# Kernel tuning notes

Hardware: AMD Instinct MI355X
Metric: run time of the kernel (lower is better)

Reference implementation:

```python
import jax, jax.numpy as jnp
import numpy as np

D_MODEL = 1024
NUM_HEADS = 16
D_HEAD = D_MODEL // NUM_HEADS
LN_EPS = 1e-5


def setup_inputs() -> dict:
    key = jax.random.key(0)
    ks = jax.random.split(key, 10)
    s = 1.0 / np.sqrt(D_MODEL)
    inp = {
        "batch": jax.random.normal(ks[0], (4, 2048, D_MODEL), dtype=jnp.float32),
        "wq": jax.random.uniform(ks[1], (D_MODEL, D_MODEL), jnp.float32, -s, s),
        "bq": jax.random.uniform(ks[2], (D_MODEL,), jnp.float32, -s, s),
        "wk": jax.random.uniform(ks[3], (D_MODEL, D_MODEL), jnp.float32, -s, s),
        "bk": jax.random.uniform(ks[4], (D_MODEL,), jnp.float32, -s, s),
        "wv": jax.random.uniform(ks[5], (D_MODEL, D_MODEL), jnp.float32, -s, s),
        "bv": jax.random.uniform(ks[6], (D_MODEL,), jnp.float32, -s, s),
        "wo": jax.random.uniform(ks[7], (D_MODEL, D_MODEL), jnp.float32, -s, s),
        "bo": jax.random.uniform(ks[8], (D_MODEL,), jnp.float32, -s, s),
        "ln_g": jnp.ones((D_MODEL,), jnp.float32),
        "ln_b": jnp.zeros((D_MODEL,), jnp.float32),
    }
    return inp


def reference(batch, wq, bq, wk, bk, wv, bv, wo, bo, ln_g, ln_b):
    B, S, D = batch.shape
    # QKV projections (torch Linear: x @ W.T + b)
    q = (batch @ wq.T + bq).reshape(B, S, NUM_HEADS, D_HEAD)
    k = (batch @ wk.T + bk).reshape(B, S, NUM_HEADS, D_HEAD)
    v = (batch @ wv.T + bv).reshape(B, S, NUM_HEADS, D_HEAD)
    # attention scores [B, H, S, S]
    scores = jnp.einsum("bqhd,bkhd->bhqk", q, k) / np.sqrt(D_HEAD).astype(np.float32)
    # (original masked_fill is not in-place -> mask has no effect; omitted)
    probs = jax.nn.softmax(scores, axis=-1)
    attn = jnp.einsum("bhqk,bkhd->bqhd", probs, v).reshape(B, S, D)
    residual = attn @ wo.T + bo  # dropout = identity (eval mode)
    x = batch + residual
    mu = jnp.mean(x, axis=-1, keepdims=True)
    var = jnp.mean(jnp.square(x - mu), axis=-1, keepdims=True)
    return (x - mu) / jnp.sqrt(var + LN_EPS) * ln_g + ln_b
```

## Files before the change

kernel.cpp:

```cpp
#include <hip/hip_runtime.h>

typedef __bf16 bf16_t;
typedef __bf16 v8bf __attribute__((ext_vector_type(8)));
typedef __bf16 v4bf __attribute__((ext_vector_type(4)));
typedef float  v4f  __attribute__((ext_vector_type(4)));

#define D_MODEL 1024
#define NHEAD   16
#define DHEAD   64
#define SEQ     2048
#define BATCH   4
#define ROWS    (BATCH*SEQ)

#define GLD16(g, l) __builtin_amdgcn_global_load_lds( \
    (const __attribute__((address_space(1))) void*)(g), \
    (__attribute__((address_space(3))) void*)(l), 16, 0, 0)

__global__ __launch_bounds__(256) void k_prep(const float* __restrict__ batch,
                                              const float* __restrict__ wq,
                                              const float* __restrict__ wk,
                                              const float* __restrict__ wv,
                                              const float* __restrict__ wo,
                                              const float* __restrict__ bq,
                                              const float* __restrict__ bk,
                                              const float* __restrict__ bv,
                                              bf16_t* __restrict__ Xb,
                                              bf16_t* __restrict__ Wqkv,
                                              bf16_t* __restrict__ Wob,
                                              float* __restrict__ bqkv) {
    int bid = blockIdx.x, t = threadIdx.x;
    const float* src; bf16_t* dst; int idx;
    if (bid < 8192)       { src = batch; dst = Xb;             idx = bid * 256 + t; }
    else if (bid < 9216)  { src = wq;    dst = Wqkv;           idx = (bid - 8192) * 256 + t; }
    else if (bid < 10240) { src = wk;    dst = Wqkv + 1048576; idx = (bid - 9216) * 256 + t; }
    else if (bid < 11264) { src = wv;    dst = Wqkv + 2097152; idx = (bid - 10240) * 256 + t; }
    else if (bid < 12288) { src = wo;    dst = Wob;            idx = (bid - 11264) * 256 + t; }
    else {
        int i = (bid - 12288) * 256 + t;
        if (i < 1024) bqkv[i] = bq[i];
        else if (i < 2048) bqkv[i] = bk[i - 1024];
        else if (i < 3072) bqkv[i] = bv[i - 2048];
        return;
    }
    float4 f = ((const float4*)src)[idx];
    v4bf o;
    o[0] = (bf16_t)f.x; o[1] = (bf16_t)f.y; o[2] = (bf16_t)f.z; o[3] = (bf16_t)f.w;
    ((v4bf*)dst)[idx] = o;
}

__global__ __launch_bounds__(256, 3) void k_gemm_bt(
    const bf16_t* __restrict__ A, const bf16_t* __restrict__ Bm,
    const float* __restrict__ bias, const float* __restrict__ resid,
    bf16_t* __restrict__ Cb, float* __restrict__ Cf,
    int M, int N, int K, int qcols, float qmul)
{
    __shared__ bf16_t As[2][128 * 32];
    __shared__ bf16_t Bs[2][128 * 32];

    int nTile = N >> 7;
    int m0 = (blockIdx.x / nTile) << 7;
    int n0 = (blockIdx.x % nTile) << 7;
    int t = threadIdx.x;
    int w = t >> 6, lane = t & 63, quad = lane >> 4, ln = lane & 15;
    int wm = (w >> 1) << 6, wn = (w & 1) << 6;

    int srow = lane >> 2;
    int scol = ((lane & 3) ^ ((lane >> 3) & 3)) << 3;
    const bf16_t* Ag0 = A  + (size_t)(m0 + w * 16 +      srow) * K + scol;
    const bf16_t* Ag1 = A  + (size_t)(m0 + w * 16 + 64 + srow) * K + scol;
    const bf16_t* Bg0 = Bm + (size_t)(n0 + w * 16 +      srow) * K + scol;
    const bf16_t* Bg1 = Bm + (size_t)(n0 + w * 16 + 64 + srow) * K + scol;
    int lo0 = (w * 16) * 32, lo1 = (w * 16 + 64) * 32;

    v4f acc[4][4];
#pragma unroll
    for (int i = 0; i < 4; i++)
#pragma unroll
        for (int j = 0; j < 4; j++) acc[i][j] = (v4f){0.f, 0.f, 0.f, 0.f};

    GLD16(Ag0, &As[0][lo0]);
    GLD16(Ag1, &As[0][lo1]);
    GLD16(Bg0, &Bs[0][lo0]);
    GLD16(Bg1, &Bs[0][lo1]);

    int sw = (ln >> 1) & 3;
    int buf = 0;
    for (int k0 = 0; k0 < K; k0 += 32, buf ^= 1) {
        __syncthreads();
        if (k0 + 32 < K) {
            GLD16(Ag0 + k0 + 32, &As[buf ^ 1][lo0]);
            GLD16(Ag1 + k0 + 32, &As[buf ^ 1][lo1]);
            GLD16(Bg0 + k0 + 32, &Bs[buf ^ 1][lo0]);
            GLD16(Bg1 + k0 + 32, &Bs[buf ^ 1][lo1]);
        }
        v8bf af[4], bfr[4];
#pragma unroll
        for (int mt = 0; mt < 4; mt++)
            af[mt] = *(const v8bf*)&As[buf][(wm + mt * 16 + ln) * 32 + ((quad ^ sw) << 3)];
#pragma unroll
        for (int nt = 0; nt < 4; nt++)
            bfr[nt] = *(const v8bf*)&Bs[buf][(wn + nt * 16 + ln) * 32 + ((quad ^ sw) << 3)];
#pragma unroll
        for (int mt = 0; mt < 4; mt++)
#pragma unroll
            for (int nt = 0; nt < 4; nt++)
                acc[mt][nt] = __builtin_amdgcn_mfma_f32_16x16x32_bf16(af[mt], bfr[nt], acc[mt][nt], 0, 0, 0);
    }

#pragma unroll
    for (int mt = 0; mt < 4; mt++) {
#pragma unroll
        for (int r = 0; r < 4; r++) {
            int row = m0 + wm + mt * 16 + quad * 4 + r;
#pragma unroll
            for (int nt = 0; nt < 4; nt++) {
                int col = n0 + wn + nt * 16 + ln;
                float v = acc[mt][nt][r] + bias[col];
                if (Cf) Cf[(size_t)row * N + col] = v + resid[(size_t)row * N + col];
                else {
                    if (col < qcols) v *= qmul;
                    Cb[(size_t)row * N + col] = (bf16_t)v;
                }
            }
        }
    }
}

__global__ __launch_bounds__(256) void k_transpose_v(const bf16_t* __restrict__ qkv,
                                                     bf16_t* __restrict__ vt) {
    __shared__ bf16_t tile[64 * 72];
    int bid = blockIdx.x;
    int st = bid & 31, bh = bid >> 5, b = bh >> 4, h = bh & 15;
    int t = threadIdx.x;
    const bf16_t* src = qkv + (size_t)(b * SEQ + st * 64) * 3072 + 2048 + h * 64;
#pragma unroll
    for (int i = 0; i < 2; i++) {
        int c = t + i * 256, row = c >> 3, c8 = (c & 7) << 3;
        *(uint4*)&tile[row * 72 + c8] = *(const uint4*)(src + (size_t)row * 3072 + c8);
    }
    __syncthreads();
    bf16_t* dst = vt + (size_t)bh * DHEAD * SEQ + st * 64;
#pragma unroll
    for (int i = 0; i < 2; i++) {
        int c = t + i * 256, d = c >> 3, s8 = (c & 7) << 3;
        v8bf o;
#pragma unroll
        for (int j = 0; j < 8; j++) o[j] = tile[(s8 + j) * 72 + d];
        *(v8bf*)(dst + (size_t)d * SEQ + s8) = o;
    }
}

__global__ __launch_bounds__(256, 3) void k_attn(const bf16_t* __restrict__ qkv,
                                                 const bf16_t* __restrict__ vt,
                                                 bf16_t* __restrict__ attn) {
    __shared__ bf16_t Ks[2][64 * 64];
    __shared__ bf16_t Vs[2][64 * 64];
    __shared__ bf16_t Pl[4][16 * 64];

    int bid = blockIdx.x;
    int qt = bid & 15, bh = bid >> 4, b = bh >> 4, h = bh & 15;
    int t = threadIdx.x, w = t >> 6, lane = t & 63, quad = lane >> 4, ln = lane & 15;
    int q0 = qt * 128 + w * 32;

    v8bf qf[2][2];
#pragma unroll
    for (int qs = 0; qs < 2; qs++) {
        const bf16_t* Qp = qkv + (size_t)(b * SEQ + q0 + qs * 16 + ln) * 3072 + h * 64 + quad * 8;
        qf[qs][0] = *(const v8bf*)Qp;
        qf[qs][1] = *(const v8bf*)(Qp + 32);
    }

    int srow = lane >> 3;
    int scol = ((lane & 7) ^ (lane >> 3)) << 3;
    const bf16_t* Kg0 = qkv + (size_t)(b * SEQ + w * 8 +      srow) * 3072 + 1024 + h * 64 + scol;
    const bf16_t* Kg1 = qkv + (size_t)(b * SEQ + w * 8 + 32 + srow) * 3072 + 1024 + h * 64 + scol;
    const bf16_t* Vg0 = vt + (size_t)bh * DHEAD * SEQ + (size_t)(w * 8 +      srow) * SEQ + scol;
    const bf16_t* Vg1 = vt + (size_t)bh * DHEAD * SEQ + (size_t)(w * 8 + 32 + srow) * SEQ + scol;
    int ko0 = (w * 8) * 64, ko1 = (w * 8 + 32) * 64;

    bf16_t* Pw = &Pl[w][0];
    int swv = ln & 7;

    v4f o[2][4];
#pragma unroll
    for (int qs = 0; qs < 2; qs++)
#pragma unroll
        for (int d = 0; d < 4; d++) o[qs][d] = (v4f){0.f, 0.f, 0.f, 0.f};
    float lsum[2][4] = {{0.f,0.f,0.f,0.f},{0.f,0.f,0.f,0.f}};

    GLD16(Kg0, &Ks[0][ko0]);
    GLD16(Kg1, &Ks[0][ko1]);
    GLD16(Vg0, &Vs[0][ko0]);
    GLD16(Vg1, &Vs[0][ko1]);

    int buf = 0;
    for (int kt = 0; kt < SEQ; kt += 64, buf ^= 1) {
        __syncthreads();
        if (kt + 64 < SEQ) {
            GLD16(Kg0 + (size_t)(kt + 64) * 3072, &Ks[buf ^ 1][ko0]);
            GLD16(Kg1 + (size_t)(kt + 64) * 3072, &Ks[buf ^ 1][ko1]);
            GLD16(Vg0 + kt + 64, &Vs[buf ^ 1][ko0]);
            GLD16(Vg1 + kt + 64, &Vs[buf ^ 1][ko1]);
        }

        v4f s0[4], s1[4];
#pragma unroll
        for (int nt = 0; nt < 4; nt++) {
            int rr = 4 * ln + nt;
            int swr = rr & 7;
            v8bf kf0 = *(const v8bf*)&Ks[buf][rr * 64 + ((quad ^ swr) << 3)];
            v8bf kf1 = *(const v8bf*)&Ks[buf][rr * 64 + (((quad + 4) ^ swr) << 3)];
            s0[nt] = (v4f){0.f, 0.f, 0.f, 0.f};
            s1[nt] = (v4f){0.f, 0.f, 0.f, 0.f};
            s0[nt] = __builtin_amdgcn_mfma_f32_16x16x32_bf16(qf[0][0], kf0, s0[nt], 0, 0, 0);
            s0[nt] = __builtin_amdgcn_mfma_f32_16x16x32_bf16(qf[0][1], kf1, s0[nt], 0, 0, 0);
            s1[nt] = __builtin_amdgcn_mfma_f32_16x16x32_bf16(qf[1][0], kf0, s1[nt], 0, 0, 0);
            s1[nt] = __builtin_amdgcn_mfma_f32_16x16x32_bf16(qf[1][1], kf1, s1[nt], 0, 0, 0);
        }

        v8bf vf[8];
#pragma unroll
        for (int d = 0; d < 4; d++) {
            vf[d * 2]     = *(const v8bf*)&Vs[buf][(d * 16 + ln) * 64 + ((quad ^ swv) << 3)];
            vf[d * 2 + 1] = *(const v8bf*)&Vs[buf][(d * 16 + ln) * 64 + (((quad + 4) ^ swv) << 3)];
        }

#pragma unroll
        for (int qs = 0; qs < 2; qs++) {
            v4f* s = qs ? s1 : s0;
#pragma unroll
            for (int r = 0; r < 4; r++) {
                float p0 = __builtin_amdgcn_exp2f(s[0][r]);
                float p1 = __builtin_amdgcn_exp2f(s[1][r]);
                float p2 = __builtin_amdgcn_exp2f(s[2][r]);
                float p3 = __builtin_amdgcn_exp2f(s[3][r]);
                int m = quad * 4 + r;
                v4bf pk;
                pk[0] = (bf16_t)p0; pk[1] = (bf16_t)p1;
                pk[2] = (bf16_t)p2; pk[3] = (bf16_t)p3;
                *(v4bf*)&Pw[m * 64 + (((ln >> 1) ^ (m & 7)) << 3) + ((ln & 1) << 2)] = pk;
                lsum[qs][r] += (p0 + p1) + (p2 + p3);
            }
#pragma unroll
            for (int tk = 0; tk < 2; tk++) {
                v8bf pf = *(const v8bf*)&Pw[ln * 64 + (((tk * 4 + quad) ^ (ln & 7)) << 3)];
#pragma unroll
                for (int d = 0; d < 4; d++)
                    o[qs][d] = __builtin_amdgcn_mfma_f32_16x16x32_bf16(pf, vf[tk + d * 2], o[qs][d], 0, 0, 0);
            }
        }
    }

#pragma unroll
    for (int qs = 0; qs < 2; qs++)
#pragma unroll
        for (int r = 0; r < 4; r++) {
#pragma unroll
            for (int off = 1; off < 16; off <<= 1) lsum[qs][r] += __shfl_xor(lsum[qs][r], off);
        }

#pragma unroll
    for (int qs = 0; qs < 2; qs++) {
        int rowg = b * SEQ + q0 + qs * 16;
#pragma unroll
        for (int r = 0; r < 4; r++) {
            float inv = 1.f / lsum[qs][r];
#pragma unroll
            for (int d = 0; d < 4; d++)
                attn[(size_t)(rowg + quad * 4 + r) * D_MODEL + h * 64 + d * 16 + ln] =
                    (bf16_t)(o[qs][d][r] * inv);
        }
    }
}

__global__ __launch_bounds__(256) void k_layernorm(const float* __restrict__ y,
                                                   const float* __restrict__ g,
                                                   const float* __restrict__ beta,
                                                   float* __restrict__ out) {
    __shared__ float rs[4], rq[4];
    int row = blockIdx.x, t = threadIdx.x;
    int w = t >> 6, lane = t & 63;
    float4 v = ((const float4*)(y + (size_t)row * D_MODEL))[t];
    float s = v.x + v.y + v.z + v.w;
    float q = v.x * v.x + v.y * v.y + v.z * v.z + v.w * v.w;
#pragma unroll
    for (int off = 1; off < 64; off <<= 1) {
        s += __shfl_xor(s, off);
        q += __shfl_xor(q, off);
    }
    if (lane == 0) { rs[w] = s; rq[w] = q; }
    __syncthreads();
    s = rs[0] + rs[1] + rs[2] + rs[3];
    q = rq[0] + rq[1] + rq[2] + rq[3];
    float mu = s * (1.f / D_MODEL);
    float var = q * (1.f / D_MODEL) - mu * mu;
    float rstd = rsqrtf(var + 1e-5f);
    float4 gg = ((const float4*)g)[t];
    float4 bb = ((const float4*)beta)[t];
    float4 o;
    o.x = (v.x - mu) * rstd * gg.x + bb.x;
    o.y = (v.y - mu) * rstd * gg.y + bb.y;
    o.z = (v.z - mu) * rstd * gg.z + bb.z;
    o.w = (v.w - mu) * rstd * gg.w + bb.w;
    ((float4*)(out + (size_t)row * D_MODEL))[t] = o;
}

extern "C" void kernel_launch(void* const* d_in, const int* in_sizes, int n_in,
                              void* d_out, int out_size, void* d_ws, size_t ws_size,
                              hipStream_t stream) {
    const float* batch = (const float*)d_in[0];
    const float* wq = (const float*)d_in[1];
    const float* bq = (const float*)d_in[2];
    const float* wk = (const float*)d_in[3];
    const float* bk = (const float*)d_in[4];
    const float* wv = (const float*)d_in[5];
    const float* bv = (const float*)d_in[6];
    const float* wo = (const float*)d_in[7];
    const float* bo = (const float*)d_in[8];
    const float* ln_g = (const float*)d_in[9];
    const float* ln_b = (const float*)d_in[10];
    float* out = (float*)d_out;

    char* ws = (char*)d_ws;
    size_t offXb   = 0;
    size_t offWqkv = offXb + (size_t)ROWS * D_MODEL * 2;
    size_t offWo   = offWqkv + (size_t)3072 * 1024 * 2;
    size_t offBias = offWo + (size_t)1024 * 1024 * 2;
    size_t offQKV  = offBias + 3072 * 4;
    size_t offAttn = offQKV + (size_t)ROWS * 3072 * 2;
    size_t total   = offAttn + (size_t)ROWS * D_MODEL * 2;
    if (ws_size < total) return;

    bf16_t* Xb   = (bf16_t*)(ws + offXb);
    bf16_t* Vt   = (bf16_t*)(ws + offXb);
    bf16_t* Wqkv = (bf16_t*)(ws + offWqkv);
    bf16_t* Wob  = (bf16_t*)(ws + offWo);
    float*  bqkv = (float*)(ws + offBias);
    bf16_t* qkv  = (bf16_t*)(ws + offQKV);
    float*  y    = (float*)(ws + offQKV);
    bf16_t* attn = (bf16_t*)(ws + offAttn);

    const float SC = 0.125f * 1.44269504088896f;

    k_prep<<<12300, 256, 0, stream>>>(batch, wq, wk, wv, wo, bq, bk, bv,
                                      Xb, Wqkv, Wob, bqkv);
    k_gemm_bt<<<64 * 24, 256, 0, stream>>>(Xb, Wqkv, bqkv, nullptr, qkv, nullptr,
                                           8192, 3072, 1024, 1024, SC);
    k_transpose_v<<<2048, 256, 0, stream>>>(qkv, Vt);
    k_attn<<<1024, 256, 0, stream>>>(qkv, Vt, attn);
    k_gemm_bt<<<64 * 8, 256, 0, stream>>>(attn, Wob, bo, batch, nullptr, y,
                                          8192, 1024, 1024, 0, 1.0f);
    k_layernorm<<<8192, 256, 0, stream>>>(y, ln_g, ln_b, out);
}
```

Before: 340.2 us.

## Compute transposed scores so P feeds PV MFMA directly from registers

Swaps the MFMA operand order so the score tile comes out transposed (keys along rows), and remaps the K row order so each lane's accumulator values line up with the A-operand layout of the PV MFMA. This removes the per-wave LDS round trip for P (store plus reload) and the Pl shared buffer. Row sums become per-lane and are reduced with a shuffle across the quads. Launch bounds drop from 3 to 2 blocks per SM, which gives more registers per thread but may lower occupancy. A dead V load is left in the loop.

```diff
diff --git a/kernel.cpp b/kernel.cpp
--- a/kernel.cpp
+++ b/kernel.cpp
@@ -150,12 +150,11 @@
     }
 }
 
-__global__ __launch_bounds__(256, 3) void k_attn(const bf16_t* __restrict__ qkv,
+__global__ __launch_bounds__(256, 2) void k_attn(const bf16_t* __restrict__ qkv,
                                                  const bf16_t* __restrict__ vt,
                                                  bf16_t* __restrict__ attn) {
     __shared__ bf16_t Ks[2][64 * 64];
     __shared__ bf16_t Vs[2][64 * 64];
-    __shared__ bf16_t Pl[4][16 * 64];
 
     int bid = blockIdx.x;
     int qt = bid & 15, bh = bid >> 4, b = bh >> 4, h = bh & 15;
@@ -178,15 +177,18 @@
     const bf16_t* Vg1 = vt + (size_t)bh * DHEAD * SEQ + (size_t)(w * 8 + 32 + srow) * SEQ + scol;
     int ko0 = (w * 8) * 64, ko1 = (w * 8 + 32) * 64;
 
-    bf16_t* Pw = &Pl[w][0];
     int swv = ln & 7;
+    int rrbase = ((ln >> 2) << 3) + (ln & 3);
+    int o0 = (rrbase) * 64,       o1 = (rrbase + 4) * 64;
+    int o2 = (rrbase + 32) * 64,  o3 = (rrbase + 36) * 64;
+    int sw0 = rrbase & 7, sw1 = (rrbase + 4) & 7;
 
     v4f o[2][4];
 #pragma unroll
     for (int qs = 0; qs < 2; qs++)
 #pragma unroll
         for (int d = 0; d < 4; d++) o[qs][d] = (v4f){0.f, 0.f, 0.f, 0.f};
-    float lsum[2][4] = {{0.f,0.f,0.f,0.f},{0.f,0.f,0.f,0.f}};
+    float lsum[2] = {0.f, 0.f};
 
     GLD16(Kg0, &Ks[0][ko0]);
     GLD16(Kg1, &Ks[0][ko1]);
@@ -203,68 +205,64 @@
             GLD16(Vg1 + kt + 64, &Vs[buf ^ 1][ko1]);
         }
 
+        const bf16_t* Kb = &Ks[buf][0];
         v4f s0[4], s1[4];
+        int rof[4] = {o0, o1, o2, o3};
+        int rsw[4] = {sw0, sw1, sw0, sw1};
 #pragma unroll
         for (int nt = 0; nt < 4; nt++) {
-            int rr = 4 * ln + nt;
-            int swr = rr & 7;
-            v8bf kf0 = *(const v8bf*)&Ks[buf][rr * 64 + ((quad ^ swr) << 3)];
-            v8bf kf1 = *(const v8bf*)&Ks[buf][rr * 64 + (((quad + 4) ^ swr) << 3)];
+            v8bf kf0 = *(const v8bf*)&Kb[rof[nt] + ((quad ^ rsw[nt]) << 3)];
+            v8bf kf1 = *(const v8bf*)&Kb[rof[nt] + (((quad + 4) ^ rsw[nt]) << 3)];
             s0[nt] = (v4f){0.f, 0.f, 0.f, 0.f};
             s1[nt] = (v4f){0.f, 0.f, 0.f, 0.f};
-            s0[nt] = __builtin_amdgcn_mfma_f32_16x16x32_bf16(qf[0][0], kf0, s0[nt], 0, 0, 0);
-            s0[nt] = __builtin_amdgcn_mfma_f32_16x16x32_bf16(qf[0][1], kf1, s0[nt], 0, 0, 0);
-            s1[nt] = __builtin_amdgcn_mfma_f32_16x16x32_bf16(qf[1][0], kf0, s1[nt], 0, 0, 0);
-            s1[nt] = __builtin_amdgcn_mfma_f32_16x16x32_bf16(qf[1][1], kf1, s1[nt], 0, 0, 0);
-        }
-
-        v8bf vf[8];
-#pragma unroll
-        for (int d = 0; d < 4; d++) {
-            vf[d * 2]     = *(const v8bf*)&Vs[buf][(d * 16 + ln) * 64 + ((quad ^ swv) << 3)];
-            vf[d * 2 + 1] = *(const v8bf*)&Vs[buf][(d * 16 + ln) * 64 + (((quad + 4) ^ swv) << 3)];
-        }
-
-#pragma unroll
-        for (int qs = 0; qs < 2; qs++) {
-            v4f* s = qs ? s1 : s0;
-#pragma unroll
-            for (int r = 0; r < 4; r++) {
-                float p0 = __builtin_amdgcn_exp2f(s[0][r]);
-                float p1 = __builtin_amdgcn_exp2f(s[1][r]);
-                float p2 = __builtin_amdgcn_exp2f(s[2][r]);
-                float p3 = __builtin_amdgcn_exp2f(s[3][r]);
-                int m = quad * 4 + r;
-                v4bf pk;
-                pk[0] = (bf16_t)p0; pk[1] = (bf16_t)p1;
-                pk[2] = (bf16_t)p2; pk[3] = (bf16_t)p3;
-                *(v4bf*)&Pw[m * 64 + (((ln >> 1) ^ (m & 7)) << 3) + ((ln & 1) << 2)] = pk;
-                lsum[qs][r] += (p0 + p1) + (p2 + p3);
+            s0[nt] = __builtin_amdgcn_mfma_f32_16x16x32_bf16(kf0, qf[0][0], s0[nt], 0, 0, 0);
+            s0[nt] = __builtin_amdgcn_mfma_f32_16x16x32_bf16(kf1, qf[0][1], s0[nt], 0, 0, 0);
+            s1[nt] = __builtin_amdgcn_mfma_f32_16x16x32_bf16(kf0, qf[1][0], s1[nt], 0, 0, 0);
+            s1[nt] = __builtin_amdgcn_mfma_f32_16x16x32_bf16(kf1, qf[1][1], s1[nt], 0, 0, 0);
+        }
+
+#pragma unroll
+        for (int tk = 0; tk < 2; tk++) {
+            v8bf vf0 = *(const v8bf*)&Vs[buf][(0 * 16 + ln) * 64 + (((tk * 4 + 0 + quad * 0) ^ 0) << 3)];
+            v8bf vfd[4];
+#pragma unroll
+            for (int d = 0; d < 4; d++)
+                vfd[d] = *(const v8bf*)&Vs[buf][(d * 16 + ln) * 64 + (((tk * 4 + quad) ^ swv) << 3)];
+            (void)vf0;
+#pragma unroll
+            for (int qs = 0; qs < 2; qs++) {
+                v4f* s = qs ? s1 : s0;
+                float e0 = __builtin_amdgcn_exp2f(s[2 * tk][0]);
+                float e1 = __builtin_amdgcn_exp2f(s[2 * tk][1]);
+                float e2 = __builtin_amdgcn_exp2f(s[2 * tk][2]);
+                float e3 = __builtin_amdgcn_exp2f(s[2 * tk][3]);
+                float e4 = __builtin_amdgcn_exp2f(s[2 * tk + 1][0]);
+                float e5 = __builtin_amdgcn_exp2f(s[2 * tk + 1][1]);
+                float e6 = __builtin_amdgcn_exp2f(s[2 * tk + 1][2]);
+                float e7 = __builtin_amdgcn_exp2f(s[2 * tk + 1][3]);
+                v8bf pf;
+                pf[0] = (bf16_t)e0; pf[1] = (bf16_t)e1; pf[2] = (bf16_t)e2; pf[3] = (bf16_t)e3;
+                pf[4] = (bf16_t)e4; pf[5] = (bf16_t)e5; pf[6] = (bf16_t)e6; pf[7] = (bf16_t)e7;
+                lsum[qs] += ((e0 + e1) + (e2 + e3)) + ((e4 + e5) + (e6 + e7));
+#pragma unroll
+                for (int d = 0; d < 4; d++)
+                    o[qs][d] = __builtin_amdgcn_mfma_f32_16x16x32_bf16(pf, vfd[d], o[qs][d], 0, 0, 0);
             }
-#pragma unroll
-            for (int tk = 0; tk < 2; tk++) {
-                v8bf pf = *(const v8bf*)&Pw[ln * 64 + (((tk * 4 + quad) ^ (ln & 7)) << 3)];
-#pragma unroll
-                for (int d = 0; d < 4; d++)
-                    o[qs][d] = __builtin_amdgcn_mfma_f32_16x16x32_bf16(pf, vf[tk + d * 2], o[qs][d], 0, 0, 0);
-            }
-        }
-    }
-
-#pragma unroll
-    for (int qs = 0; qs < 2; qs++)
-#pragma unroll
-        for (int r = 0; r < 4; r++) {
-#pragma unroll
-            for (int off = 1; off < 16; off <<= 1) lsum[qs][r] += __shfl_xor(lsum[qs][r], off);
-        }
+        }
+    }
+
+#pragma unroll
+    for (int qs = 0; qs < 2; qs++) {
+        lsum[qs] += __shfl_xor(lsum[qs], 16);
+        lsum[qs] += __shfl_xor(lsum[qs], 32);
+    }
 
 #pragma unroll
     for (int qs = 0; qs < 2; qs++) {
         int rowg = b * SEQ + q0 + qs * 16;
 #pragma unroll
         for (int r = 0; r < 4; r++) {
-            float inv = 1.f / lsum[qs][r];
+            float inv = 1.f / __shfl(lsum[qs], 20 * quad + r);
 #pragma unroll
             for (int d = 0; d < 4; d++)
                 attn[(size_t)(rowg + quad * 4 + r) * D_MODEL + h * 64 + d * 16 + ln] =
```

After: 314.5 us. 1.08x faster.
